# Optimization experiments

Hardware: AMD Instinct MI355X
Metric: run time of the kernel (lower is better)

Reference implementation:

```python
import jax, jax.numpy as jnp
import numpy as np
import math

VOCAB, D, H, NL, L, B = 50257, 768, 12, 4, 1024, 2
DH = D // H
DFF = 4 * D
ALPHA = 0.25
NEG = -1e9


def _ln(x, g, b, eps=1e-5):
    mu = x.mean(-1, keepdims=True)
    var = ((x - mu) ** 2).mean(-1, keepdims=True)
    return (x - mu) * jax.lax.rsqrt(var + eps) * g + b


def setup_inputs() -> dict:
    key = jax.random.key(0)
    ks = jax.random.split(key, 16)
    s = 0.02
    tokens = jax.random.randint(ks[0], (B, L), 0, VOCAB)
    timelike_mask = jax.random.randint(ks[1], (NL, D), 0, 2).astype(jnp.int32)
    embed = jax.random.normal(ks[2], (VOCAB, D), jnp.float32) * s
    pos_emb = jax.random.normal(ks[3], (L, D), jnp.float32) * s
    wq = jax.random.normal(ks[4], (NL, D, D), jnp.float32) * s
    wk = jax.random.normal(ks[5], (NL, D, D), jnp.float32) * s
    wv = jax.random.normal(ks[6], (NL, D, D), jnp.float32) * s
    wo = jax.random.normal(ks[7], (NL, D, D), jnp.float32) * s
    ff_w1 = jax.random.normal(ks[8], (NL, DFF, D), jnp.float32) * s
    ff_b1 = jnp.zeros((NL, DFF), jnp.float32)
    ff_w2 = jax.random.normal(ks[9], (NL, D, DFF), jnp.float32) * s
    ff_b2 = jnp.zeros((NL, D), jnp.float32)
    ln1_g = jnp.ones((NL, D), jnp.float32); ln1_b = jnp.zeros((NL, D), jnp.float32)
    ln2_g = jnp.ones((NL, D), jnp.float32); ln2_b = jnp.zeros((NL, D), jnp.float32)
    lnf_g = jnp.ones((D,), jnp.float32); lnf_b = jnp.zeros((D,), jnp.float32)
    return dict(tokens=tokens, timelike_mask=timelike_mask, embed=embed, pos_emb=pos_emb,
                wq=wq, wk=wk, wv=wv, wo=wo,
                ln1_g=ln1_g, ln1_b=ln1_b, ln2_g=ln2_g, ln2_b=ln2_b,
                ff_w1=ff_w1, ff_b1=ff_b1, ff_w2=ff_w2, ff_b2=ff_b2,
                lnf_g=lnf_g, lnf_b=lnf_b)


def reference(tokens, timelike_mask, embed, pos_emb, wq, wk, wv, wo,
              ln1_g, ln1_b, ln2_g, ln2_b, ff_w1, ff_b1, ff_w2, ff_b2,
              lnf_g, lnf_b):
    Bc, Lc = tokens.shape
    scale = math.sqrt(DH)
    # embeddings: token + learned position
    h = embed[tokens] + pos_emb[None, :Lc]  # (B,L,D)
    # additive causal mask, matching torch's -inf attention_mask convention
    causal = jnp.where(jnp.tril(jnp.ones((Lc, Lc), bool)), 0.0, NEG)[None, None]  # (1,1,L,L)
    for i in range(NL):
        xn = _ln(h, ln1_g[i], ln1_b[i])
        # nn.Linear(bias=False): y = x @ W.T, W is (out,in)
        q = jnp.einsum('bld,od->blo', xn, wq[i]).reshape(Bc, Lc, H, DH).astype(jnp.float32)
        k = jnp.einsum('bld,od->blo', xn, wk[i]).reshape(Bc, Lc, H, DH).astype(jnp.float32)
        v = jnp.einsum('bld,od->blo', xn, wv[i]).reshape(Bc, Lc, H, DH)
        # Minkowski term: scores_std - 2*alpha*(Q*P_t)K^T  ==  (Q*(1-2*alpha*m)) K^T
        m = timelike_mask[i].astype(jnp.float32).reshape(H, DH)  # per-head timelike directions
        q_eff = q * (1.0 - 2.0 * ALPHA * m)[None, None]
        scores = jnp.einsum('bqhd,bkhd->bhqk', q_eff, k) / scale + causal
        aw = jax.nn.softmax(scores, axis=-1)  # dropout=0 (eval)
        attn = jnp.einsum('bhqk,bkhd->bqhd', aw, v).reshape(Bc, Lc, D)
        h = h + jnp.einsum('bld,od->blo', attn, wo[i])
        xn2 = _ln(h, ln2_g[i], ln2_b[i])
        ff = jax.nn.gelu(jnp.einsum('bld,fd->blf', xn2, ff_w1[i]) + ff_b1[i], approximate=False)
        h = h + jnp.einsum('blf,df->bld', ff, ff_w2[i]) + ff_b2[i]
    h = _ln(h, lnf_g, lnf_b)
    logits = jnp.einsum('bld,vd->blv', h, embed)  # tied LM head
    return logits
```

## Files before the change

### kernel.cpp

```cpp
#include <hip/hip_runtime.h>
#include <math.h>

#define VOCABSZ 50257
#define VPAD 50432
#define DMODEL 768
#define NHEAD 12
#define NLAYER 4
#define SEQ 1024
#define BATCH 2
#define DHEAD 64
#define DFFN 3072
#define BT (BATCH * SEQ)
#define NBH (BATCH * NHEAD)

typedef __attribute__((ext_vector_type(8))) short bf16x8;
typedef __attribute__((ext_vector_type(4))) float f32x4;

__device__ __forceinline__ ushort f2bf(float f) {
  uint u = __builtin_bit_cast(uint, f);
  u = (u + 0x7fffu + ((u >> 16) & 1u)) >> 16;
  return (ushort)u;
}

__device__ __forceinline__ float bf2f(ushort u) {
  uint x = ((uint)u) << 16;
  return __builtin_bit_cast(float, x);
}

__device__ __forceinline__ void gl_lds16(const ushort* g, ushort* l) {
  __builtin_amdgcn_global_load_lds(
      (const __attribute__((address_space(1))) void*)g,
      (__attribute__((address_space(3))) void*)l, 16, 0, 0);
}

__global__ __launch_bounds__(256) void conv_qkv3_kernel(
    const float* __restrict__ wq, const float* __restrict__ wk,
    const float* __restrict__ wv, ushort* __restrict__ dst) {
  const int per4 = DMODEL * DMODEL / 4;
  const int total = NLAYER * per4;
  int i = blockIdx.x * 256 + threadIdx.x;
  if (i >= 3 * total) return;
  int which = i / total;
  int rem = i - which * total;
  const float* src = (which == 0) ? wq : (which == 1) ? wk : wv;
  int layer = rem / per4, r2 = rem % per4;
  float4 v = reinterpret_cast<const float4*>(src)[rem];
  reinterpret_cast<ushort4*>(dst)[(size_t)layer * (3 * per4) + which * per4 +
                                  r2] =
      make_ushort4(f2bf(v.x), f2bf(v.y), f2bf(v.z), f2bf(v.w));
}

__global__ __launch_bounds__(256) void conv3_kernel(
    const float* __restrict__ wo, ushort* __restrict__ wo_b,
    const float* __restrict__ fw1, ushort* __restrict__ fw1_b,
    const float* __restrict__ fw2, ushort* __restrict__ fw2_b) {
  const int n1 = NLAYER * DMODEL * DMODEL / 4;
  const int nf = NLAYER * DFFN * DMODEL / 4;
  int i = blockIdx.x * 256 + threadIdx.x;
  const float* src;
  ushort* dst;
  int idx;
  if (i < n1) {
    src = wo; dst = wo_b; idx = i;
  } else if (i < n1 + nf) {
    src = fw1; dst = fw1_b; idx = i - n1;
  } else if (i < n1 + 2 * nf) {
    src = fw2; dst = fw2_b; idx = i - n1 - nf;
  } else {
    return;
  }
  float4 v = reinterpret_cast<const float4*>(src)[idx];
  reinterpret_cast<ushort4*>(dst)[idx] =
      make_ushort4(f2bf(v.x), f2bf(v.y), f2bf(v.z), f2bf(v.w));
}

__global__ __launch_bounds__(256) void conv_embed_kernel(
    const float* __restrict__ emb, ushort* __restrict__ dst) {
  int i = blockIdx.x * 256 + threadIdx.x;
  if (i >= VPAD * DMODEL / 4) return;
  int row = (i * 4) / DMODEL;
  ushort4 o = make_ushort4(0, 0, 0, 0);
  if (row < VOCABSZ) {
    float4 v = reinterpret_cast<const float4*>(emb)[i];
    o = make_ushort4(f2bf(v.x), f2bf(v.y), f2bf(v.z), f2bf(v.w));
  }
  reinterpret_cast<ushort4*>(dst)[i] = o;
}

template <int KS, bool RBIAS, bool EMB>
__global__ __launch_bounds__(256) void ln_kernel(
    float* __restrict__ h, const ushort* __restrict__ part,
    const float* __restrict__ rb, const int* __restrict__ tok,
    const float* __restrict__ emb, const float* __restrict__ pos,
    const float* __restrict__ g, const float* __restrict__ bta,
    ushort* __restrict__ o) {
  __shared__ float red[8];
  int row = blockIdx.x;
  int tid = threadIdx.x;
  float* xr = h + (size_t)row * DMODEL;
  const float* er = nullptr;
  const float* pr = nullptr;
  if (EMB) {
    er = emb + (size_t)tok[row] * DMODEL;
    pr = pos + (size_t)(row & (SEQ - 1)) * DMODEL;
  }
  float v[3];
  float s = 0.f, sq = 0.f;
#pragma unroll
  for (int j = 0; j < 3; ++j) {
    int c = tid + j * 256;
    float a;
    if (EMB) {
      a = er[c] + pr[c];
      xr[c] = a;
    } else {
      a = xr[c];
      if (RBIAS) a += rb[c];
      if (KS > 0) {
#pragma unroll
        for (int z = 0; z < KS; ++z)
          a += bf2f(part[(size_t)z * BT * DMODEL + (size_t)row * DMODEL + c]);
        xr[c] = a;
      }
    }
    v[j] = a;
    s += a;
    sq += a * a;
  }
#pragma unroll
  for (int off = 1; off < 64; off <<= 1) {
    s += __shfl_xor(s, off);
    sq += __shfl_xor(sq, off);
  }
  int wid = tid >> 6;
  if ((tid & 63) == 0) { red[wid * 2] = s; red[wid * 2 + 1] = sq; }
  __syncthreads();
  float S = red[0] + red[2] + red[4] + red[6];
  float SQ = red[1] + red[3] + red[5] + red[7];
  float mu = S * (1.0f / DMODEL);
  float var = SQ * (1.0f / DMODEL) - mu * mu;
  float r = rsqrtf(var + 1e-5f);
  ushort* orow = o + (size_t)row * DMODEL;
#pragma unroll
  for (int j = 0; j < 3; ++j) {
    int c = tid + j * 256;
    orow[c] = f2bf((v[j] - mu) * r * g[c] + bta[c]);
  }
}

__global__ __launch_bounds__(256) void fattn_kernel(
    const ushort* __restrict__ q, const ushort* __restrict__ k,
    const ushort* __restrict__ vt, ushort* __restrict__ o) {
  __shared__ __align__(16) ushort Ks[2][64 * 64];
  __shared__ __align__(16) ushort Vs[2][64 * 64];
  __shared__ __align__(16) ushort Ps[4][16][80];
  const int bid = blockIdx.x;
  const int wgid = (bid & 7) * 48 + (bid >> 3);
  const int z = wgid / 16, qb_ = wgid % 16;
  const int b = z / NHEAD, hh = z % NHEAD;
  const int q0 = (15 - qb_) * 64;
  const int tid = threadIdx.x, w = tid >> 6, l = tid & 63;
  const int fr = l & 15, ks = l >> 4;
  const int qrow = q0 + w * 16 + fr;
  const ushort* qp = q + (size_t)(b * SEQ + qrow) * DMODEL + hh * DHEAD;
  const bf16x8 qf0 = *reinterpret_cast<const bf16x8*>(qp + ks * 8);
  const bf16x8 qf1 = *reinterpret_cast<const bf16x8*>(qp + 32 + ks * 8);

  const int srow = w * 16 + (l >> 3);
  const int g0 = ((l & 7) ^ (srow & 7)) * 8;

  auto stage = [&](int k0, int d) {
#pragma unroll
    for (int c = 0; c < 2; ++c) {
      int r = srow + c * 8;
      gl_lds16(k + (size_t)(b * SEQ + k0 + r) * DMODEL + hh * DHEAD + g0,
               &Ks[d][(w * 16 + c * 8) * 64]);
      gl_lds16(vt + (size_t)(z * 64 + r) * SEQ + k0 + g0,
               &Vs[d][(w * 16 + c * 8) * 64]);
    }
  };

  f32x4 acc_o[4] = {};
  float mrun = -1e30f, lrun = 0.f;
  const int nt = q0 >> 6;

  stage(0, 0);
  for (int t = 0; t <= nt; ++t) {
    const int cur = t & 1;
    if (t < nt) {
      stage((t + 1) * 64, cur ^ 1);
      asm volatile("s_waitcnt vmcnt(4)" ::: "memory");
    } else {
      asm volatile("s_waitcnt vmcnt(0)" ::: "memory");
    }
    __builtin_amdgcn_s_barrier();
    __builtin_amdgcn_sched_barrier(0);
    f32x4 acc_s[4] = {};
#pragma unroll
    for (int kstep = 0; kstep < 2; ++kstep) {
      const bf16x8 qf = kstep ? qf1 : qf0;
#pragma unroll
      for (int kb = 0; kb < 4; ++kb) {
        int ra = kb * 16 + fr;
        bf16x8 af = *reinterpret_cast<const bf16x8*>(
            &Ks[cur][ra * 64 + (((kstep * 4 + ks) ^ (ra & 7)) * 8)]);
        acc_s[kb] =
            __builtin_amdgcn_mfma_f32_16x16x32_bf16(af, qf, acc_s[kb], 0, 0, 0);
      }
    }
    const bool diag = (t == nt);
    float pm = -1e30f;
    float sv[4][4];
#pragma unroll
    for (int kb = 0; kb < 4; ++kb)
#pragma unroll
      for (int r = 0; r < 4; ++r) {
        float s = acc_s[kb][r];
        if (diag && (q0 + kb * 16 + ks * 4 + r > qrow)) s = -1e30f;
        sv[kb][r] = s;
        pm = fmaxf(pm, s);
      }
    pm = fmaxf(pm, __shfl_xor(pm, 16));
    pm = fmaxf(pm, __shfl_xor(pm, 32));
    if (!__all(pm - mrun <= 8.0f)) {
      float mnew = fmaxf(mrun, pm);
      float scale = __expf(mrun - mnew);
      lrun *= scale;
#pragma unroll
      for (int db = 0; db < 4; ++db) acc_o[db] *= scale;
      mrun = mnew;
    }
    float psum = 0.f;
#pragma unroll
    for (int kb = 0; kb < 4; ++kb) {
      float p0 = __expf(sv[kb][0] - mrun);
      float p1 = __expf(sv[kb][1] - mrun);
      float p2 = __expf(sv[kb][2] - mrun);
      float p3 = __expf(sv[kb][3] - mrun);
      psum += (p0 + p1) + (p2 + p3);
      *reinterpret_cast<ushort4*>(&Ps[w][fr][kb * 16 + ks * 4]) =
          make_ushort4(f2bf(p0), f2bf(p1), f2bf(p2), f2bf(p3));
    }
    psum += __shfl_xor(psum, 16);
    psum += __shfl_xor(psum, 32);
    lrun += psum;
#pragma unroll
    for (int kstep = 0; kstep < 2; ++kstep) {
      bf16x8 pf =
          *reinterpret_cast<const bf16x8*>(&Ps[w][fr][kstep * 32 + ks * 8]);
#pragma unroll
      for (int db = 0; db < 4; ++db) {
        int rd = db * 16 + fr;
        bf16x8 vf = *reinterpret_cast<const bf16x8*>(
            &Vs[cur][rd * 64 + (((kstep * 4 + ks) ^ (rd & 7)) * 8)]);
        acc_o[db] =
            __builtin_amdgcn_mfma_f32_16x16x32_bf16(vf, pf, acc_o[db], 0, 0, 0);
      }
    }
    __builtin_amdgcn_sched_barrier(0);
    __builtin_amdgcn_s_barrier();
  }
  float rinv = 1.0f / lrun;
#pragma unroll
  for (int db = 0; db < 4; ++db) {
    ushort4 o4 =
        make_ushort4(f2bf(acc_o[db][0] * rinv), f2bf(acc_o[db][1] * rinv),
                     f2bf(acc_o[db][2] * rinv), f2bf(acc_o[db][3] * rinv));
    *reinterpret_cast<ushort4*>(o + (size_t)(b * SEQ + qrow) * DMODEL +
                                hh * DHEAD + db * 16 + ks * 4) = o4;
  }
}

template <bool QKV, bool BIAS, bool GELU, bool RES, bool OUTBF, bool SWZ,
          bool PART>
__global__ __launch_bounds__(256) void gemm_bf16_nt(
    const ushort* __restrict__ A, const ushort* __restrict__ B,
    const float* __restrict__ bias, const int* __restrict__ tmask,
    const float* __restrict__ res, float* __restrict__ Cf,
    ushort* __restrict__ Cb, int ldc, ushort* __restrict__ qb,
    ushort* __restrict__ kb, ushort* __restrict__ vt, int M, int K, int Nreal,
    int kchunk) {
  __shared__ __align__(16) ushort As[2][128 * 32];
  __shared__ __align__(16) ushort Bs[2][128 * 32];
  int bnx, bmy;
  if (SWZ) {
    int bid = blockIdx.x;
    int chunk = gridDim.x >> 3;
    int wgid = (bid & 7) * chunk + (bid >> 3);
    int mb = M >> 7;
    bmy = wgid % mb;
    bnx = wgid / mb;
  } else {
    bnx = blockIdx.x;
    bmy = blockIdx.y;
  }
  const int m0 = bmy * 128, n0 = bnx * 128;
  const int kbeg = PART ? blockIdx.z * kchunk : 0;
  const int kend = PART ? kbeg + kchunk : K;
  if (PART) Cb += (size_t)blockIdx.z * M * ldc;
  const int tid = threadIdx.x;
  const int w = tid >> 6, l = tid & 63;
  const int wr = w >> 1, wc = w & 1;
  const int fr = l & 15, ks = l >> 4;

  const int seg0 = w * 2, seg1 = w * 2 + 1;
  const int srow0 = seg0 * 16 + (l >> 2);
  const int srow1 = seg1 * 16 + (l >> 2);
  const int koff0 = (((l & 3) ^ ((srow0 >> 1) & 3))) * 8;
  const int koff1 = (((l & 3) ^ ((srow1 >> 1) & 3))) * 8;
  const ushort* A0 = A + (size_t)(m0 + srow0) * K + koff0;
  const ushort* A1 = A + (size_t)(m0 + srow1) * K + koff1;
  const ushort* B0 = B + (size_t)(n0 + srow0) * K + koff0;
  const ushort* B1 = B + (size_t)(n0 + srow1) * K + koff1;

  int aoff[4], boff[4];
#pragma unroll
  for (int i = 0; i < 4; ++i) {
    int ra = wr * 64 + i * 16 + fr;
    aoff[i] = ra * 32 + ((ks ^ ((ra >> 1) & 3)) * 8);
    int rb = wc * 64 + i * 16 + fr;
    boff[i] = rb * 32 + ((ks ^ ((rb >> 1) & 3)) * 8);
  }

  gl_lds16(A0 + kbeg, &As[0][seg0 * 512]);
  gl_lds16(A1 + kbeg, &As[0][seg1 * 512]);
  gl_lds16(B0 + kbeg, &Bs[0][seg0 * 512]);
  gl_lds16(B1 + kbeg, &Bs[0][seg1 * 512]);

  f32x4 acc[4][4] = {};
  int cur = 0;
  for (int k0 = kbeg; k0 < kend; k0 += 32) {
    const int nxt = k0 + 32;
    if (nxt < kend) {
      gl_lds16(A0 + nxt, &As[cur ^ 1][seg0 * 512]);
      gl_lds16(A1 + nxt, &As[cur ^ 1][seg1 * 512]);
      gl_lds16(B0 + nxt, &Bs[cur ^ 1][seg0 * 512]);
      gl_lds16(B1 + nxt, &Bs[cur ^ 1][seg1 * 512]);
      asm volatile("s_waitcnt vmcnt(4)" ::: "memory");
    } else {
      asm volatile("s_waitcnt vmcnt(0)" ::: "memory");
    }
    __builtin_amdgcn_s_barrier();
    __builtin_amdgcn_sched_barrier(0);
    bf16x8 af[4], bfr[4];
#pragma unroll
    for (int i = 0; i < 4; ++i)
      af[i] = *reinterpret_cast<const bf16x8*>(&As[cur][aoff[i]]);
#pragma unroll
    for (int i = 0; i < 4; ++i)
      bfr[i] = *reinterpret_cast<const bf16x8*>(&Bs[cur][boff[i]]);
#pragma unroll
    for (int mi = 0; mi < 4; ++mi)
#pragma unroll
      for (int nj = 0; nj < 4; ++nj)
        acc[mi][nj] = __builtin_amdgcn_mfma_f32_16x16x32_bf16(
            af[mi], bfr[nj], acc[mi][nj], 0, 0, 0);
    __builtin_amdgcn_sched_barrier(0);
    __builtin_amdgcn_s_barrier();
    cur ^= 1;
  }

#pragma unroll
  for (int mi = 0; mi < 4; ++mi) {
#pragma unroll
    for (int nj = 0; nj < 4; ++nj) {
      int n = n0 + wc * 64 + nj * 16 + fr;
      if (n < Nreal) {
        if (PART) {
#pragma unroll
          for (int r = 0; r < 4; ++r) {
            int m = m0 + wr * 64 + mi * 16 + ks * 4 + r;
            Cb[(size_t)m * ldc + n] = f2bf(acc[mi][nj][r]);
          }
        } else if (QKV) {
          if (n < DMODEL) {
            float sc = (1.0f - 0.5f * (float)tmask[n]) * 0.125f;
#pragma unroll
            for (int r = 0; r < 4; ++r) {
              int m = m0 + wr * 64 + mi * 16 + ks * 4 + r;
              qb[(size_t)m * DMODEL + n] = f2bf(acc[mi][nj][r] * sc);
            }
          } else if (n < 2 * DMODEL) {
#pragma unroll
            for (int r = 0; r < 4; ++r) {
              int m = m0 + wr * 64 + mi * 16 + ks * 4 + r;
              kb[(size_t)m * DMODEL + (n - DMODEL)] = f2bf(acc[mi][nj][r]);
            }
          } else {
            int d = n - 2 * DMODEL;
            int key = (m0 & (SEQ - 1)) + wr * 64 + mi * 16 + ks * 4;
            size_t zr = (size_t)((m0 >> 10) * NHEAD + (d >> 6)) * 64 + (d & 63);
            ushort4 p4 = make_ushort4(
                f2bf(acc[mi][nj][0]), f2bf(acc[mi][nj][1]),
                f2bf(acc[mi][nj][2]), f2bf(acc[mi][nj][3]));
            *reinterpret_cast<ushort4*>(vt + zr * SEQ + key) = p4;
          }
        } else {
#pragma unroll
          for (int r = 0; r < 4; ++r) {
            int m = m0 + wr * 64 + mi * 16 + ks * 4 + r;
            float v = acc[mi][nj][r];
            if (BIAS) v += bias[n];
            if (GELU) v = 0.5f * v * (1.0f + erff(v * 0.70710678118f));
            if (RES) v += res[(size_t)m * ldc + n];
            if (OUTBF)
              Cb[(size_t)m * ldc + n] = f2bf(v);
            else
              Cf[(size_t)m * ldc + n] = v;
          }
        }
      }
    }
  }
}

__global__ __launch_bounds__(512, 2) void gemm_lmhead(
    const ushort* __restrict__ A, const ushort* __restrict__ B,
    float* __restrict__ C) {
  __shared__ __align__(16) ushort SMEM[4 * 256 * 64];
  const int K = DMODEL;
  const int NTILE = K / 64;
  const int ITERS = NTILE / 2;

  const int bid = blockIdx.x;
  const int chunk = gridDim.x >> 3;
  const int wgid = (bid & 7) * chunk + (bid >> 3);
  const int m0 = (wgid & 7) * 256;
  const int n0 = (wgid >> 3) * 256;

  const int tid = threadIdx.x;
  const int w = tid >> 6, l = tid & 63;
  const int wr = w >> 2, wc = w & 3;
  const int fr = l & 15, ks = l >> 4;

  const int strow = tid >> 3;
  const int stk = ((tid & 7) ^ (strow & 7)) * 8;
  const int wseg = (w << 3) * 64;

  const int fsw0 = (ks ^ (fr & 7)) * 8;
  const int fsw1 = ((4 | ks) ^ (fr & 7)) * 8;
  const int arow = (wr * 128 + fr) * 64;
  const int brow = (wc * 64 + fr) * 64;

  bf16x8 Ar[4][2], Br[4][2];
  f32x4 acc[8][4] = {};

#define STA(d, kt, rb)                                            \
  gl_lds16(A + (size_t)(m0 + (rb) + strow) * K + (kt) * 64 + stk, \
           SMEM + (d) * 16384 + (rb) * 64 + wseg)
#define STB(d, kt, rb)                                            \
  gl_lds16(B + (size_t)(n0 + (rb) + strow) * K + (kt) * 64 + stk, \
           SMEM + 32768 + (d) * 16384 + (rb) * 64 + wseg)
#define RDA(d, mi, kst)                           \
  (*reinterpret_cast<const bf16x8*>(              \
      &SMEM[(d) * 16384 + arow + (mi) * 1024 + ((kst) ? fsw1 : fsw0)]))
#define RDB(d, nj, kst)                           \
  (*reinterpret_cast<const bf16x8*>(              \
      &SMEM[32768 + (d) * 16384 + brow + (nj) * 1024 + ((kst) ? fsw1 : fsw0)]))
#define MMAQ(mh, nh)                                                       \
  _Pragma("unroll") for (int kst = 0; kst < 2; ++kst)                      \
  _Pragma("unroll") for (int mi = 0; mi < 4; ++mi)                         \
  _Pragma("unroll") for (int nj = 0; nj < 2; ++nj)                         \
    acc[(mh)*4 + mi][(nh)*2 + nj] = __builtin_amdgcn_mfma_f32_16x16x32_bf16( \
        Ar[mi][kst], Br[(nh)*2 + nj][kst], acc[(mh)*4 + mi][(nh)*2 + nj],  \
        0, 0, 0)
#define BAR __builtin_amdgcn_s_barrier()
#define PRIO1 __builtin_amdgcn_s_setprio(1)
#define PRIO0 __builtin_amdgcn_s_setprio(0)

  STA(0, 0, 0); STA(0, 0, 64); STA(0, 0, 128); STA(0, 0, 192);
  STB(0, 0, 0); STB(0, 0, 64); STB(0, 0, 128); STB(0, 0, 192);
  STB(1, 1, 0); STB(1, 1, 64); STB(1, 1, 128); STB(1, 1, 192);
  asm volatile("s_waitcnt vmcnt(4)" ::: "memory");
  BAR;

  for (int it = 0; it < ITERS; ++it) {
    const int t1 = 2 * it + 1;
    const int tn = 2 * it + 2;
    const bool s0 = tn < NTILE, s1 = tn + 1 < NTILE;
#pragma unroll
    for (int mi = 0; mi < 4; ++mi) {
      Ar[mi][0] = RDA(0, mi, 0); Ar[mi][1] = RDA(0, mi, 1);
    }
#pragma unroll
    for (int nj = 0; nj < 2; ++nj) {
      Br[nj][0] = RDB(0, nj, 0); Br[nj][1] = RDB(0, nj, 1);
    }
    STA(1, t1, 0); STA(1, t1, 64);
    BAR; PRIO1; MMAQ(0, 0); PRIO0; BAR;
#pragma unroll
    for (int nj = 2; nj < 4; ++nj) {
      Br[nj][0] = RDB(0, nj, 0); Br[nj][1] = RDB(0, nj, 1);
    }
    STA(1, t1, 128); STA(1, t1, 192);
    BAR; PRIO1; MMAQ(0, 1); PRIO0; BAR;
#pragma unroll
    for (int mi = 0; mi < 4; ++mi) {
      Ar[mi][0] = RDA(0, mi + 4, 0); Ar[mi][1] = RDA(0, mi + 4, 1);
    }
    if (s0) { STB(0, tn, 0); STB(0, tn, 64); }
    BAR; PRIO1; MMAQ(1, 1); PRIO0; BAR;
    if (s0) { STB(0, tn, 128); STB(0, tn, 192); }
    BAR; PRIO1; MMAQ(1, 0); PRIO0;
    if (s0)
      asm volatile("s_waitcnt vmcnt(4)" ::: "memory");
    else
      asm volatile("s_waitcnt vmcnt(0)" ::: "memory");
    BAR;
#pragma unroll
    for (int mi = 0; mi < 4; ++mi) {
      Ar[mi][0] = RDA(1, mi, 0); Ar[mi][1] = RDA(1, mi, 1);
    }
#pragma unroll
    for (int nj = 0; nj < 2; ++nj) {
      Br[nj][0] = RDB(1, nj, 0); Br[nj][1] = RDB(1, nj, 1);
    }
    if (s0) { STA(0, tn, 0); STA(0, tn, 64); }
    BAR; PRIO1; MMAQ(0, 0); PRIO0; BAR;
#pragma unroll
    for (int nj = 2; nj < 4; ++nj) {
      Br[nj][0] = RDB(1, nj, 0); Br[nj][1] = RDB(1, nj, 1);
    }
    if (s0) { STA(0, tn, 128); STA(0, tn, 192); }
    BAR; PRIO1; MMAQ(0, 1); PRIO0; BAR;
#pragma unroll
    for (int mi = 0; mi < 4; ++mi) {
      Ar[mi][0] = RDA(1, mi + 4, 0); Ar[mi][1] = RDA(1, mi + 4, 1);
    }
    if (s1) { STB(1, tn + 1, 0); STB(1, tn + 1, 64); }
    BAR; PRIO1; MMAQ(1, 1); PRIO0; BAR;
    if (s1) { STB(1, tn + 1, 128); STB(1, tn + 1, 192); }
    BAR; PRIO1; MMAQ(1, 0); PRIO0;
    if (it + 1 < ITERS) {
      asm volatile("s_waitcnt vmcnt(4)" ::: "memory");
      BAR;
    }
  }

  float* eb = reinterpret_cast<float*>(SMEM);
#pragma unroll 1
  for (int p = 0; p < 2; ++p) {
    __syncthreads();
    if (wr == p) {
#pragma unroll
      for (int mi = 0; mi < 8; ++mi)
#pragma unroll
        for (int nj = 0; nj < 4; ++nj)
#pragma unroll
          for (int r = 0; r < 4; ++r)
            eb[(mi * 16 + ks * 4 + r) * 256 + wc * 64 + nj * 16 + fr] =
                acc[mi][nj][r];
    }
    __syncthreads();
    const size_t rowbase = (size_t)(m0 + p * 128) * VOCABSZ + n0;
#pragma unroll 8
    for (int c = 0; c < 64; ++c) {
      int lin = c * 512 + tid;
      int row = lin >> 8, col = lin & 255;
      if (n0 + col < VOCABSZ) {
        __builtin_nontemporal_store(
            eb[lin], C + rowbase + (size_t)row * VOCABSZ + col);
      }
    }
  }
#undef STA
#undef STB
#undef RDA
#undef RDB
#undef MMAQ
#undef BAR
#undef PRIO1
#undef PRIO0
}

extern "C" void kernel_launch(void* const* d_in, const int* in_sizes, int n_in,
                              void* d_out, int out_size, void* d_ws,
                              size_t ws_size, hipStream_t stream) {
  const int* tokens = (const int*)d_in[0];
  const int* tmask = (const int*)d_in[1];
  const float* embed = (const float*)d_in[2];
  const float* pos = (const float*)d_in[3];
  const float* wq = (const float*)d_in[4];
  const float* wk = (const float*)d_in[5];
  const float* wv = (const float*)d_in[6];
  const float* wo = (const float*)d_in[7];
  const float* ln1g = (const float*)d_in[8];
  const float* ln1b = (const float*)d_in[9];
  const float* ln2g = (const float*)d_in[10];
  const float* ln2b = (const float*)d_in[11];
  const float* fw1 = (const float*)d_in[12];
  const float* fb1 = (const float*)d_in[13];
  const float* fw2 = (const float*)d_in[14];
  const float* fb2 = (const float*)d_in[15];
  const float* lnfg = (const float*)d_in[16];
  const float* lnfb = (const float*)d_in[17];

  char* wp = (char*)d_ws;
  auto alloc = [&](size_t bytes) {
    void* p = wp;
    wp += (bytes + 255) & ~(size_t)255;
    return p;
  };
  float* h = (float*)alloc((size_t)BT * DMODEL * 4);
  ushort* part = (ushort*)alloc((size_t)8 * BT * DMODEL * 2);
  ushort* qb = (ushort*)alloc((size_t)BT * DMODEL * 2);
  ushort* kb = (ushort*)alloc((size_t)BT * DMODEL * 2);
  ushort* vt = (ushort*)alloc((size_t)NBH * DHEAD * SEQ * 2);
  ushort* xn = (ushort*)alloc((size_t)BT * DMODEL * 2);
  ushort* ab = (ushort*)alloc((size_t)BT * DMODEL * 2);
  ushort* ffb = (ushort*)alloc((size_t)BT * DFFN * 2);
  ushort* wqkv_b = (ushort*)alloc((size_t)NLAYER * 3 * DMODEL * DMODEL * 2);
  ushort* wo_b = (ushort*)alloc((size_t)NLAYER * DMODEL * DMODEL * 2);
  ushort* fw1_b = (ushort*)alloc((size_t)NLAYER * DFFN * DMODEL * 2);
  ushort* fw2_b = (ushort*)alloc((size_t)NLAYER * DMODEL * DFFN * 2);
  ushort* emb_b = (ushort*)alloc((size_t)VPAD * DMODEL * 2);

  const int per4 = DMODEL * DMODEL / 4;
  const int nff4 = NLAYER * DFFN * DMODEL / 4;
  conv_qkv3_kernel<<<(3 * NLAYER * per4 + 255) / 256, 256, 0, stream>>>(
      wq, wk, wv, wqkv_b);
  conv3_kernel<<<(NLAYER * per4 + 2 * nff4 + 255) / 256, 256, 0, stream>>>(
      wo, wo_b, fw1, fw1_b, fw2, fw2_b);
  conv_embed_kernel<<<(VPAD * DMODEL / 4 + 255) / 256, 256, 0, stream>>>(
      embed, emb_b);

  const dim3 gqkv(3 * DMODEL / 128, BT / 128);
  const dim3 gff(DFFN / 128, BT / 128);
  const dim3 gwo(DMODEL / 128, BT / 128, 4);
  const dim3 gff2(DMODEL / 128, BT / 128, 8);

  for (int i = 0; i < NLAYER; ++i) {
    if (i == 0)
      ln_kernel<0, false, true><<<BT, 256, 0, stream>>>(
          h, nullptr, nullptr, tokens, embed, pos, ln1g, ln1b, xn);
    else
      ln_kernel<8, true, false><<<BT, 256, 0, stream>>>(
          h, part, fb2 + (i - 1) * DMODEL, nullptr, nullptr, nullptr,
          ln1g + i * DMODEL, ln1b + i * DMODEL, xn);

    gemm_bf16_nt<true, false, false, false, false, false, false>
        <<<gqkv, 256, 0, stream>>>(
            xn, wqkv_b + (size_t)i * 3 * DMODEL * DMODEL, nullptr,
            tmask + i * DMODEL, nullptr, nullptr, nullptr, 0, qb, kb, vt, BT,
            DMODEL, 3 * DMODEL, DMODEL);

    fattn_kernel<<<NBH * (SEQ / 64), 256, 0, stream>>>(qb, kb, vt, ab);

    gemm_bf16_nt<false, false, false, false, false, false, true>
        <<<gwo, 256, 0, stream>>>(
            ab, wo_b + (size_t)i * DMODEL * DMODEL, nullptr, nullptr, nullptr,
            nullptr, part, DMODEL, nullptr, nullptr, nullptr, BT, DMODEL,
            DMODEL, DMODEL / 4);

    ln_kernel<4, false, false><<<BT, 256, 0, stream>>>(
        h, part, nullptr, nullptr, nullptr, nullptr, ln2g + i * DMODEL,
        ln2b + i * DMODEL, xn);

    gemm_bf16_nt<false, true, true, false, true, false, false>
        <<<gff, 256, 0, stream>>>(
            xn, fw1_b + (size_t)i * DFFN * DMODEL, fb1 + i * DFFN, nullptr,
            nullptr, nullptr, ffb, DFFN, nullptr, nullptr, nullptr, BT, DMODEL,
            DFFN, DMODEL);

    gemm_bf16_nt<false, false, false, false, false, false, true>
        <<<gff2, 256, 0, stream>>>(
            ffb, fw2_b + (size_t)i * DMODEL * DFFN, nullptr, nullptr, nullptr,
            nullptr, part, DMODEL, nullptr, nullptr, nullptr, BT, DFFN, DMODEL,
            DFFN / 8);
  }

  ln_kernel<8, true, false><<<BT, 256, 0, stream>>>(
      h, part, fb2 + (NLAYER - 1) * DMODEL, nullptr, nullptr, nullptr, lnfg,
      lnfb, xn);

  gemm_lmhead<<<8 * (VPAD / 256), 512, 0, stream>>>(xn, emb_b, (float*)d_out);
}
```

Baseline: 839.7 us.

## Split flash attention along the key dimension with a separate merge kernel

Each (batch, head, query-block) attention workgroup is split into two halves over key tiles, which doubles the grid to give more parallelism and better load balance on the causal triangle. Each half writes unnormalized fp32 partial outputs plus running max and sum. A new merge kernel combines them with log-sum-exp rescaling and writes bf16. This adds an extra kernel launch and fp32 partial traffic through global memory each layer.

```diff
diff --git a/kernel.cpp b/kernel.cpp
--- a/kernel.cpp
+++ b/kernel.cpp
@@ -150,18 +150,38 @@
 
 __global__ __launch_bounds__(256) void fattn_kernel(
     const ushort* __restrict__ q, const ushort* __restrict__ k,
-    const ushort* __restrict__ vt, ushort* __restrict__ o) {
+    const ushort* __restrict__ vt, float* __restrict__ Opart,
+    float* __restrict__ ml) {
   __shared__ __align__(16) ushort Ks[2][64 * 64];
   __shared__ __align__(16) ushort Vs[2][64 * 64];
   __shared__ __align__(16) ushort Ps[4][16][80];
   const int bid = blockIdx.x;
-  const int wgid = (bid & 7) * 48 + (bid >> 3);
-  const int z = wgid / 16, qb_ = wgid % 16;
+  const int wgid = (bid & 7) * 96 + (bid >> 3);
+  const int z = wgid / 32;
+  const int rem = wgid % 32;
+  const int qb_ = rem >> 1, s = rem & 1;
   const int b = z / NHEAD, hh = z % NHEAD;
   const int q0 = (15 - qb_) * 64;
+  const int tcnt = (q0 >> 6) + 1;
+  const int half0 = (tcnt + 1) >> 1;
+  const int tbeg = s ? half0 : 0;
+  const int tend = s ? tcnt : half0;
   const int tid = threadIdx.x, w = tid >> 6, l = tid & 63;
   const int fr = l & 15, ks = l >> 4;
   const int qrow = q0 + w * 16 + fr;
+  const size_t ri = (size_t)z * SEQ + qrow;
+  const size_t R = (size_t)NBH * SEQ;
+  const size_t off = (s ? R : 0) + ri;
+
+  if (tbeg >= tend) {
+    f32x4 zero = {};
+#pragma unroll
+    for (int db = 0; db < 4; ++db)
+      *reinterpret_cast<f32x4*>(Opart + off * 64 + db * 16 + ks * 4) = zero;
+    if (ks == 0) { ml[off * 2] = -1e30f; ml[off * 2 + 1] = 0.f; }
+    return;
+  }
+
   const ushort* qp = q + (size_t)(b * SEQ + qrow) * DMODEL + hh * DHEAD;
   const bf16x8 qf0 = *reinterpret_cast<const bf16x8*>(qp + ks * 8);
   const bf16x8 qf1 = *reinterpret_cast<const bf16x8*>(qp + 32 + ks * 8);
@@ -182,12 +202,11 @@
 
   f32x4 acc_o[4] = {};
   float mrun = -1e30f, lrun = 0.f;
-  const int nt = q0 >> 6;
-
-  stage(0, 0);
-  for (int t = 0; t <= nt; ++t) {
-    const int cur = t & 1;
-    if (t < nt) {
+
+  stage(tbeg * 64, 0);
+  for (int t = tbeg; t < tend; ++t) {
+    const int cur = (t - tbeg) & 1;
+    if (t + 1 < tend) {
       stage((t + 1) * 64, cur ^ 1);
       asm volatile("s_waitcnt vmcnt(4)" ::: "memory");
     } else {
@@ -208,17 +227,17 @@
             __builtin_amdgcn_mfma_f32_16x16x32_bf16(af, qf, acc_s[kb], 0, 0, 0);
       }
     }
-    const bool diag = (t == nt);
+    const bool diag = (t == tcnt - 1);
     float pm = -1e30f;
     float sv[4][4];
 #pragma unroll
     for (int kb = 0; kb < 4; ++kb)
 #pragma unroll
       for (int r = 0; r < 4; ++r) {
-        float s = acc_s[kb][r];
-        if (diag && (q0 + kb * 16 + ks * 4 + r > qrow)) s = -1e30f;
-        sv[kb][r] = s;
-        pm = fmaxf(pm, s);
+        float sc = acc_s[kb][r];
+        if (diag && (t * 64 + kb * 16 + ks * 4 + r > qrow)) sc = -1e30f;
+        sv[kb][r] = sc;
+        pm = fmaxf(pm, sc);
       }
     pm = fmaxf(pm, __shfl_xor(pm, 16));
     pm = fmaxf(pm, __shfl_xor(pm, 32));
@@ -260,15 +279,29 @@
     __builtin_amdgcn_sched_barrier(0);
     __builtin_amdgcn_s_barrier();
   }
-  float rinv = 1.0f / lrun;
-#pragma unroll
-  for (int db = 0; db < 4; ++db) {
-    ushort4 o4 =
-        make_ushort4(f2bf(acc_o[db][0] * rinv), f2bf(acc_o[db][1] * rinv),
-                     f2bf(acc_o[db][2] * rinv), f2bf(acc_o[db][3] * rinv));
-    *reinterpret_cast<ushort4*>(o + (size_t)(b * SEQ + qrow) * DMODEL +
-                                hh * DHEAD + db * 16 + ks * 4) = o4;
-  }
+#pragma unroll
+  for (int db = 0; db < 4; ++db)
+    *reinterpret_cast<f32x4*>(Opart + off * 64 + db * 16 + ks * 4) = acc_o[db];
+  if (ks == 0) { ml[off * 2] = mrun; ml[off * 2 + 1] = lrun; }
+}
+
+__global__ __launch_bounds__(256) void fmerge_kernel(
+    const float* __restrict__ Opart, const float* __restrict__ ml,
+    ushort* __restrict__ o) {
+  int ri = blockIdx.x * 4 + (threadIdx.x >> 6);
+  int d = threadIdx.x & 63;
+  int z = ri >> 10, qrow = ri & (SEQ - 1);
+  int b = z / NHEAD, hh = z % NHEAD;
+  const size_t R = (size_t)NBH * SEQ;
+  float m0 = ml[(size_t)ri * 2], l0 = ml[(size_t)ri * 2 + 1];
+  float m1 = ml[(R + ri) * 2], l1 = ml[(R + ri) * 2 + 1];
+  float M = fmaxf(m0, m1);
+  float e0 = __expf(m0 - M), e1 = __expf(m1 - M);
+  float L = l0 * e0 + l1 * e1;
+  float v0 = Opart[(size_t)ri * 64 + d];
+  float v1 = Opart[(R + ri) * 64 + d];
+  float v = (v0 * e0 + v1 * e1) / L;
+  o[(size_t)(b * SEQ + qrow) * DMODEL + hh * DHEAD + d] = f2bf(v);
 }
 
 template <bool QKV, bool BIAS, bool GELU, bool RES, bool OUTBF, bool SWZ,
@@ -603,6 +636,8 @@
   };
   float* h = (float*)alloc((size_t)BT * DMODEL * 4);
   ushort* part = (ushort*)alloc((size_t)8 * BT * DMODEL * 2);
+  float* opart = (float*)alloc((size_t)2 * NBH * SEQ * DHEAD * 4);
+  float* mlb = (float*)alloc((size_t)2 * NBH * SEQ * 2 * 4);
   ushort* qb = (ushort*)alloc((size_t)BT * DMODEL * 2);
   ushort* kb = (ushort*)alloc((size_t)BT * DMODEL * 2);
   ushort* vt = (ushort*)alloc((size_t)NBH * DHEAD * SEQ * 2);
@@ -644,7 +679,9 @@
             tmask + i * DMODEL, nullptr, nullptr, nullptr, 0, qb, kb, vt, BT,
             DMODEL, 3 * DMODEL, DMODEL);
 
-    fattn_kernel<<<NBH * (SEQ / 64), 256, 0, stream>>>(qb, kb, vt, ab);
+    fattn_kernel<<<2 * NBH * (SEQ / 64), 256, 0, stream>>>(qb, kb, vt, opart,
+                                                           mlb);
+    fmerge_kernel<<<NBH * SEQ / 4, 256, 0, stream>>>(opart, mlb, ab);
 
     gemm_bf16_nt<false, false, false, false, false, false, true>
         <<<gwo, 256, 0, stream>>>(
```

Result: no change. 838.1 us, median of 2 (-0.2%).
